# Kernel optimization log

Hardware: AMD Instinct MI355X
Metric: run time of the kernel (lower is better)

The kernel has to match this reference:

```python
import jax, jax.numpy as jnp
import numpy as np

NUM_CLASSES = 19
EPS = 1e-8  # torch cosine_similarity eps


def setup_inputs() -> dict:
    key = jax.random.key(0)
    k1, k2 = jax.random.split(key)
    inputs = jax.random.normal(k1, (8, 256, 128, 128), dtype=jnp.float32)  # (B, D, H, W)
    targets = jax.random.randint(k2, (8, 128, 128), 0, NUM_CLASSES)        # (B, H, W)
    return {"inputs": inputs, "targets": targets}


def reference(inputs, targets):
    B, D, H, W = inputs.shape
    C = NUM_CLASSES
    # (N, D) pixel embeddings and (N,) labels
    feats = jnp.transpose(inputs, (0, 2, 3, 1)).reshape(-1, D)
    labels = targets.reshape(-1)

    # per-class centroids: sum of embeddings / max(count, 1)  (matches sum_pixel = max(mask.sum(), 1))
    counts = jax.ops.segment_sum(jnp.ones(labels.shape, jnp.float32), labels, num_segments=C)  # (C,)
    sums = jax.ops.segment_sum(feats, labels, num_segments=C)                                   # (C, D)
    centers = sums / jnp.maximum(counts, 1.0)[:, None]
    present = counts > 0  # classes absent from the batch are skipped in both loss terms

    # ---- sim_loss: sum over present classes of mean_{pixels of class i} (1 - cos(center_i, feat)) ----
    cen_px = centers[labels]                                   # (N, D)
    dot = jnp.sum(feats * cen_px, axis=1)
    n_f = jnp.sqrt(jnp.sum(feats * feats, axis=1))
    n_c = jnp.sqrt(jnp.sum(cen_px * cen_px, axis=1))
    cos_px = dot / jnp.maximum(n_f * n_c, EPS)
    per_class = jax.ops.segment_sum(1.0 - cos_px, labels, num_segments=C) / jnp.maximum(counts, 1.0)
    sim_loss = jnp.sum(jnp.where(present, per_class, 0.0))

    # ---- diff_loss: for each present i, mean_j over all C classes of
    #      (1 - cos(center_j, center_i)) if j == i else relu(cos(center_j, center_i)) ----
    n_cen = jnp.sqrt(jnp.sum(centers * centers, axis=1))       # (C,)
    S = (centers @ centers.T) / jnp.maximum(n_cen[:, None] * n_cen[None, :], EPS)  # (C, C)
    eye = jnp.eye(C, dtype=bool)
    per_pair = jnp.where(eye, 1.0 - S, jnp.maximum(S, 0.0))    # row i = losses vs class i
    per_i = jnp.mean(per_pair, axis=1)                          # mean reduction over C rows
    diff_loss = jnp.sum(jnp.where(present, per_i, 0.0))

    return jnp.reshape(diff_loss + sim_loss, (1,))  # torch returns a shape-(1,) tensor
```

## Files before the change

### kernel.cpp

```cpp
#include <hip/hip_runtime.h>
#include <math.h>

#define D_DIM 256
#define HW 16384
#define C 19
#define N_PX 131072
#define EPS 1e-8f

#define S_SC  1048576.0f
#define IS_S  (1.0f/1048576.0f)
#define U_SC  16777216.0f
#define IS_U  (1.0f/16777216.0f)

#define OFF_S    0
#define OFF_U    4864
#define OFF_CNT  9728
#define WS_ZERO  9760
#define OFF_PART 9760
#define PSTRIDE  9760
#define G1       512

__global__ __launch_bounds__(512, 4) void k1_pass(const float* __restrict__ in,
                                                  const int* __restrict__ tgt,
                                                  int* __restrict__ wsi) {
    __shared__ int sS[C * 257];
    __shared__ int sU[C * 257];
    __shared__ int s_cnt[C];
    const int tid = threadIdx.x;
    const int dq  = tid & 15;
    const int qq  = tid >> 4;

    for (int i = tid; i < C * 257; i += 512) { sS[i] = 0; sU[i] = 0; }
    if (tid < C) s_cnt[tid] = 0;
    if (blockIdx.x < 20) {
        int i = (blockIdx.x << 9) + tid;
        if (i < WS_ZERO) wsi[i] = 0;
    }
    __syncthreads();

    const int px0 = blockIdx.x << 8;
    const int b   = px0 >> 14;
    const float* bbase = in + (((size_t)(b * D_DIM + dq)) << 14);

    #pragma unroll
    for (int r = 0; r < 2; ++r) {
        const int hwq = (px0 & (HW - 1)) + (r << 7) + (qq << 2);
        const int p   = px0 + (r << 7) + (qq << 2);
        const int4 lab = *(const int4*)(tgt + p);
        if (dq == 0) {
            atomicAdd(&s_cnt[lab.x], 1); atomicAdd(&s_cnt[lab.y], 1);
            atomicAdd(&s_cnt[lab.z], 1); atomicAdd(&s_cnt[lab.w], 1);
        }

        const float* base = bbase + hwq;
        float4 v[16];
        #pragma unroll
        for (int g = 0; g < 16; ++g)
            v[g] = *(const float4*)(base + ((size_t)g << 18));

        float4 nf = {0.f, 0.f, 0.f, 0.f};
        #pragma unroll
        for (int g = 0; g < 16; ++g) {
            nf.x += v[g].x * v[g].x; nf.y += v[g].y * v[g].y;
            nf.z += v[g].z * v[g].z; nf.w += v[g].w * v[g].w;
        }
        #pragma unroll
        for (int m = 1; m <= 8; m <<= 1) {
            nf.x += __shfl_xor(nf.x, m, 64);
            nf.y += __shfl_xor(nf.y, m, 64);
            nf.z += __shfl_xor(nf.z, m, 64);
            nf.w += __shfl_xor(nf.w, m, 64);
        }
        const float sa = nf.x > 0.f ? U_SC / sqrtf(nf.x) : 0.f;
        const float sb = nf.y > 0.f ? U_SC / sqrtf(nf.y) : 0.f;
        const float sc = nf.z > 0.f ? U_SC / sqrtf(nf.z) : 0.f;
        const float sd = nf.w > 0.f ? U_SC / sqrtf(nf.w) : 0.f;

        const int rowa = lab.x * 257, rowb = lab.y * 257,
                  rowc = lab.z * 257, rowd = lab.w * 257;
        #pragma unroll
        for (int g = 0; g < 16; ++g) {
            const int dd = (g << 4) + dq;
            atomicAdd(&sS[rowa + dd], __float2int_rn(v[g].x * S_SC));
            atomicAdd(&sS[rowb + dd], __float2int_rn(v[g].y * S_SC));
            atomicAdd(&sS[rowc + dd], __float2int_rn(v[g].z * S_SC));
            atomicAdd(&sS[rowd + dd], __float2int_rn(v[g].w * S_SC));
            atomicAdd(&sU[rowa + dd], __float2int_rn(v[g].x * sa));
            atomicAdd(&sU[rowb + dd], __float2int_rn(v[g].y * sb));
            atomicAdd(&sU[rowc + dd], __float2int_rn(v[g].z * sc));
            atomicAdd(&sU[rowd + dd], __float2int_rn(v[g].w * sd));
        }
    }
    __syncthreads();

    int* __restrict__ row = wsi + OFF_PART + (size_t)blockIdx.x * PSTRIDE;
    for (int i = tid; i < C * 256; i += 512) {
        int c = i >> 8, d = i & 255;
        row[OFF_S + i] = sS[c * 257 + d];
        row[OFF_U + i] = sU[c * 257 + d];
    }
    if (tid < C)                 row[OFF_CNT + tid] = s_cnt[tid];
    else if (tid < 32)           row[OFF_CNT + tid] = 0;
}

__global__ __launch_bounds__(256) void k1b_reduce(int* __restrict__ wsi) {
    const int col4 = blockIdx.x * 256 + threadIdx.x;
    if (col4 >= PSTRIDE / 4) return;
    const int4* base = (const int4*)(wsi + OFF_PART)
                     + (size_t)blockIdx.y * 16 * (PSTRIDE / 4) + col4;
    int4 acc = {0, 0, 0, 0};
    #pragma unroll
    for (int r = 0; r < 16; ++r) {
        int4 v = base[(size_t)r * (PSTRIDE / 4)];
        acc.x += v.x; acc.y += v.y; acc.z += v.z; acc.w += v.w;
    }
    atomicAdd(&wsi[col4 * 4 + 0], acc.x);
    atomicAdd(&wsi[col4 * 4 + 1], acc.y);
    atomicAdd(&wsi[col4 * 4 + 2], acc.z);
    atomicAdd(&wsi[col4 * 4 + 3], acc.w);
}

__global__ __launch_bounds__(512) void k2_final(const int* __restrict__ wsi,
                                                float* __restrict__ out) {
    __shared__ __align__(16) float s_cen[C * 260];
    __shared__ __align__(16) float s_u[C * 260];
    __shared__ float s_nc[C];
    __shared__ float s_cntf[C];
    __shared__ float s_pair[C * C];
    __shared__ float s_sim[C];
    const int tid = threadIdx.x;

    if (tid < C) s_cntf[tid] = (float)wsi[OFF_CNT + tid];
    __syncthreads();
    for (int i = tid; i < C * 256; i += 512) {
        int c = i >> 8, d = i & 255;
        float icnt = 1.f / fmaxf(s_cntf[c], 1.f);
        s_cen[c * 260 + d] = (float)wsi[OFF_S + i] * IS_S * icnt;
        s_u[c * 260 + d]   = (float)wsi[OFF_U + i] * IS_U;
    }
    __syncthreads();
    if (tid < C) {
        float nsq = 0.f;
        for (int d = 0; d < D_DIM; ++d) {
            float x = s_cen[tid * 260 + d];
            nsq += x * x;
        }
        s_nc[tid] = sqrtf(nsq);
    }
    __syncthreads();
    if (tid < C * C) {
        int i = tid / C, j = tid % C;
        const float4* ci = (const float4*)&s_cen[i * 260];
        const float4* cj = (const float4*)&s_cen[j * 260];
        float dot = 0.f;
        #pragma unroll 8
        for (int k = 0; k < 64; ++k) {
            float4 a = ci[k], bb = cj[k];
            dot += a.x * bb.x + a.y * bb.y + a.z * bb.z + a.w * bb.w;
        }
        float S = dot / fmaxf(s_nc[i] * s_nc[j], EPS);
        s_pair[tid] = (i == j) ? (1.f - S) : fmaxf(S, 0.f);
    } else if (tid >= 384 && tid < 384 + C) {
        int i = tid - 384;
        const float4* ci = (const float4*)&s_cen[i * 260];
        const float4* ui = (const float4*)&s_u[i * 260];
        float dot = 0.f;
        #pragma unroll 8
        for (int k = 0; k < 64; ++k) {
            float4 a = ci[k], bb = ui[k];
            dot += a.x * bb.x + a.y * bb.y + a.z * bb.z + a.w * bb.w;
        }
        s_sim[i] = (s_cntf[i] > 0.f)
                 ? (1.f - dot / fmaxf(s_nc[i] * s_cntf[i], EPS)) : 0.f;
    }
    __syncthreads();
    if (tid < C) {
        float row = 0.f;
        for (int j = 0; j < C; ++j) row += s_pair[tid * C + j];
        s_pair[tid * C] = (s_cntf[tid] > 0.f) ? (row * (1.f / (float)C)) : 0.f;
    }
    __syncthreads();
    if (tid == 0) {
        float tot = 0.f;
        for (int i = 0; i < C; ++i) tot += s_pair[i * C] + s_sim[i];
        out[0] = tot;
    }
}

extern "C" void kernel_launch(void* const* d_in, const int* in_sizes, int n_in,
                              void* d_out, int out_size, void* d_ws, size_t ws_size,
                              hipStream_t stream) {
    const float* in  = (const float*)d_in[0];
    const int*   tgt = (const int*)d_in[1];
    float* out = (float*)d_out;
    int*   wsi = (int*)d_ws;

    k1_pass<<<G1, 512, 0, stream>>>(in, tgt, wsi);
    k1b_reduce<<<dim3(10, 32), 256, 0, stream>>>(wsi);
    k2_final<<<1, 512, 0, stream>>>(wsi, out);
}
```

Baseline: 216.7 us.

## Remap k1 threads so each wave covers 32 channels over 128 pixels

Each wave now owns 32 consecutive channels and each lane two adjacent pixels, instead of 16 channel groups per wave with 4 pixels per lane. Global loads become float2 reads that are contiguous across lanes. Per-pixel norms are now reduced through a shared-memory buffer with an extra barrier in place of wave shuffles. The aim is to change the LDS atomic conflict pattern (lanes in a wave hit different class rows but the same channel) and the load coalescing, at the cost of more registers (32 float2) and added block synchronisation.

```diff
diff --git a/kernel.cpp b/kernel.cpp
--- a/kernel.cpp
+++ b/kernel.cpp
@@ -26,9 +26,10 @@
     __shared__ int sS[C * 257];
     __shared__ int sU[C * 257];
     __shared__ int s_cnt[C];
+    __shared__ float s_nfp[128 * 9];
     const int tid = threadIdx.x;
-    const int dq  = tid & 15;
-    const int qq  = tid >> 4;
+    const int w   = tid >> 6;
+    const int ln  = tid & 63;
 
     for (int i = tid; i < C * 257; i += 512) { sS[i] = 0; sU[i] = 0; }
     if (tid < C) s_cnt[tid] = 0;
@@ -40,58 +41,56 @@
 
     const int px0 = blockIdx.x << 8;
     const int b   = px0 >> 14;
-    const float* bbase = in + (((size_t)(b * D_DIM + dq)) << 14);
+    const float* bbase = in + (((size_t)(b * D_DIM + (w << 5))) << 14)
+                            + (px0 & (HW - 1));
 
     #pragma unroll
     for (int r = 0; r < 2; ++r) {
-        const int hwq = (px0 & (HW - 1)) + (r << 7) + (qq << 2);
-        const int p   = px0 + (r << 7) + (qq << 2);
-        const int4 lab = *(const int4*)(tgt + p);
-        if (dq == 0) {
-            atomicAdd(&s_cnt[lab.x], 1); atomicAdd(&s_cnt[lab.y], 1);
-            atomicAdd(&s_cnt[lab.z], 1); atomicAdd(&s_cnt[lab.w], 1);
-        }
-
-        const float* base = bbase + hwq;
-        float4 v[16];
-        #pragma unroll
-        for (int g = 0; g < 16; ++g)
-            v[g] = *(const float4*)(base + ((size_t)g << 18));
-
-        float4 nf = {0.f, 0.f, 0.f, 0.f};
-        #pragma unroll
-        for (int g = 0; g < 16; ++g) {
-            nf.x += v[g].x * v[g].x; nf.y += v[g].y * v[g].y;
-            nf.z += v[g].z * v[g].z; nf.w += v[g].w * v[g].w;
-        }
-        #pragma unroll
-        for (int m = 1; m <= 8; m <<= 1) {
-            nf.x += __shfl_xor(nf.x, m, 64);
-            nf.y += __shfl_xor(nf.y, m, 64);
-            nf.z += __shfl_xor(nf.z, m, 64);
-            nf.w += __shfl_xor(nf.w, m, 64);
-        }
-        const float sa = nf.x > 0.f ? U_SC / sqrtf(nf.x) : 0.f;
-        const float sb = nf.y > 0.f ? U_SC / sqrtf(nf.y) : 0.f;
-        const float sc = nf.z > 0.f ? U_SC / sqrtf(nf.z) : 0.f;
-        const float sd = nf.w > 0.f ? U_SC / sqrtf(nf.w) : 0.f;
-
-        const int rowa = lab.x * 257, rowb = lab.y * 257,
-                  rowc = lab.z * 257, rowd = lab.w * 257;
-        #pragma unroll
-        for (int g = 0; g < 16; ++g) {
-            const int dd = (g << 4) + dq;
-            atomicAdd(&sS[rowa + dd], __float2int_rn(v[g].x * S_SC));
-            atomicAdd(&sS[rowb + dd], __float2int_rn(v[g].y * S_SC));
-            atomicAdd(&sS[rowc + dd], __float2int_rn(v[g].z * S_SC));
-            atomicAdd(&sS[rowd + dd], __float2int_rn(v[g].w * S_SC));
-            atomicAdd(&sU[rowa + dd], __float2int_rn(v[g].x * sa));
-            atomicAdd(&sU[rowb + dd], __float2int_rn(v[g].y * sb));
-            atomicAdd(&sU[rowc + dd], __float2int_rn(v[g].z * sc));
-            atomicAdd(&sU[rowd + dd], __float2int_rn(v[g].w * sd));
-        }
-    }
-    __syncthreads();
+        const int pp = (r << 7) + (ln << 1);
+        const int2 lab = *(const int2*)(tgt + px0 + pp);
+        const int la = lab.x, lb = lab.y;
+        if (w == 0) { atomicAdd(&s_cnt[la], 1); atomicAdd(&s_cnt[lb], 1); }
+
+        float2 v[32];
+        #pragma unroll
+        for (int cc = 0; cc < 32; ++cc)
+            v[cc] = *(const float2*)(bbase + ((size_t)cc << 14) + pp);
+
+        const int rowa = la * 257, rowb = lb * 257;
+
+        #pragma unroll
+        for (int cc = 0; cc < 32; ++cc) {
+            const int dd = (w << 5) + cc;
+            atomicAdd(&sS[rowa + dd], __float2int_rn(v[cc].x * S_SC));
+            atomicAdd(&sS[rowb + dd], __float2int_rn(v[cc].y * S_SC));
+        }
+
+        float na = 0.f, nb = 0.f;
+        #pragma unroll
+        for (int cc = 0; cc < 32; ++cc) {
+            na += v[cc].x * v[cc].x;
+            nb += v[cc].y * v[cc].y;
+        }
+        s_nfp[(pp - (r << 7)) * 9 + w]     = na;
+        s_nfp[(pp - (r << 7) + 1) * 9 + w] = nb;
+        __syncthreads();
+        float sumA = 0.f, sumB = 0.f;
+        #pragma unroll
+        for (int ww = 0; ww < 8; ++ww) {
+            sumA += s_nfp[(ln << 1) * 9 + ww];
+            sumB += ((ln << 1) + 1) * 9 + ww >= 0 ? s_nfp[((ln << 1) + 1) * 9 + ww] : 0.f;
+        }
+        const float sa = sumA > 0.f ? U_SC / sqrtf(sumA) : 0.f;
+        const float sb = sumB > 0.f ? U_SC / sqrtf(sumB) : 0.f;
+
+        #pragma unroll
+        for (int cc = 0; cc < 32; ++cc) {
+            const int dd = (w << 5) + cc;
+            atomicAdd(&sU[rowa + dd], __float2int_rn(v[cc].x * sa));
+            atomicAdd(&sU[rowb + dd], __float2int_rn(v[cc].y * sb));
+        }
+        __syncthreads();
+    }
 
     int* __restrict__ row = wsi + OFF_PART + (size_t)blockIdx.x * PSTRIDE;
     for (int i = tid; i < C * 256; i += 512) {
```

Result: slower. 224.0 us (+3.4%).
